# Optimization experiments

Hardware: AMD Instinct MI355X
Metric: run time of the kernel (lower is better)

## Reference

```python
import jax, jax.numpy as jnp
import numpy as np

D_MODEL, D_KEY, N_HEADS = 256, 32, 8
B, T1, T2 = 4, 2048, 2048


def setup_inputs() -> dict:
    key = jax.random.key(0)
    ks = jax.random.split(key, 12)
    s = 1.0 / np.sqrt(D_MODEL)
    inp = {
        "key_input": jax.random.normal(ks[0], (B, T1, D_MODEL), jnp.float32),
        "query_input": jax.random.normal(ks[1], (B, T2, D_MODEL), jnp.float32),
        "value_input": jax.random.normal(ks[2], (B, T1, D_MODEL), jnp.float32),
        "attention_mask": jnp.ones((B, T1, T2), dtype=jnp.bool_),  # unused by the module, kept for API fidelity
        "WK_w": jax.random.uniform(ks[3], (D_KEY * N_HEADS, D_MODEL), jnp.float32, -s, s),
        "WK_b": jax.random.uniform(ks[4], (D_KEY * N_HEADS,), jnp.float32, -s, s),
        "WQ_w": jax.random.uniform(ks[5], (D_KEY * N_HEADS, D_MODEL), jnp.float32, -s, s),
        "WQ_b": jax.random.uniform(ks[6], (D_KEY * N_HEADS,), jnp.float32, -s, s),
        "WV_w": jax.random.uniform(ks[7], (D_MODEL * N_HEADS, D_MODEL), jnp.float32, -s, s),
        "WV_b": jax.random.uniform(ks[8], (D_MODEL * N_HEADS,), jnp.float32, -s, s),
        "WO_w": jax.random.uniform(ks[9], (D_MODEL, D_MODEL * N_HEADS), jnp.float32, -1.0 / np.sqrt(D_MODEL * N_HEADS), 1.0 / np.sqrt(D_MODEL * N_HEADS)),
        "WO_b": jax.random.uniform(ks[10], (D_MODEL,), jnp.float32, -1.0 / np.sqrt(D_MODEL * N_HEADS), 1.0 / np.sqrt(D_MODEL * N_HEADS)),
    }
    return inp


def reference(key_input, query_input, value_input, attention_mask,
              WK_w, WK_b, WQ_w, WQ_b, WV_w, WV_b, WO_w, WO_b):
    b, t1, dm = key_input.shape
    t2 = query_input.shape[1]
    h, dk = N_HEADS, D_KEY
    # projections
    k = key_input @ WK_w.T + WK_b      # [b, t1, h*dk]
    q = query_input @ WQ_w.T + WQ_b    # [b, t2, h*dk]
    v = value_input @ WV_w.T + WV_b    # [b, t1, h*dm] (per-head value dim == d_model)
    # head split: channel index c = head*dk + feat (head outer), matching torch reshapes
    k = k.reshape(b, t1, h, dk)
    q = q.reshape(b, t2, h, dk)
    v = v.reshape(b, t1, h, dm)
    # scores: NO 1/sqrt(dk) scaling and NO masking (faithful to source; mask arg unused)
    scores = jnp.einsum('bshk,bqhk->bhsq', k, q)      # [b, h, t1, t2]
    attn = jax.nn.softmax(scores, axis=2)             # softmax over KEY axis (torch dim=1 of [t1,t2])
    emb = jnp.einsum('bshd,bhsq->bqdh', v, attn)      # [b, t2, dm, h]
    emb = emb.reshape(b, t2, dm * h)                  # flatten (d_model outer, head inner)
    return emb @ WO_w.T + WO_b                        # [b, t2, d_model]
```

## Files before the change

### kernel.cpp

```cpp
#include <hip/hip_runtime.h>

typedef __attribute__((ext_vector_type(8))) short short8;
typedef __attribute__((ext_vector_type(4))) short short4v;
typedef __attribute__((ext_vector_type(4))) float float4v;

constexpr int T  = 2048;
constexpr int DM = 256;
constexpr int DK = 32;

__device__ inline short f2bf(float f) {
  unsigned u = __builtin_bit_cast(unsigned, f);
  u += 0x7fff + ((u >> 16) & 1);
  return (short)(u >> 16);
}

__device__ inline short8 load8_bf(const float* __restrict__ p) {
  float4v a = *(const float4v*)p;
  float4v b = *(const float4v*)(p + 4);
  short8 r;
  r[0] = f2bf(a[0]); r[1] = f2bf(a[1]); r[2] = f2bf(a[2]); r[3] = f2bf(a[3]);
  r[4] = f2bf(b[0]); r[5] = f2bf(b[1]); r[6] = f2bf(b[2]); r[7] = f2bf(b[3]);
  return r;
}
__device__ inline short8 load8_bf(const short* __restrict__ p) {
  return *(const short8*)p;
}
__device__ inline void storeC(short* C, long idx, float v) { C[idx] = f2bf(v); }
__device__ inline void storeC(float* C, long idx, float v) { C[idx] = v; }

template<typename TA, typename TB, typename TC, int MODE>
__global__ __launch_bounds__(256)
void gemm_nt(const TA* __restrict__ A, const TB* __restrict__ Bw,
             const float* __restrict__ bias, TC* __restrict__ C,
             int M, int N, int K) {
  __shared__ __align__(16) short As[128][40];
  __shared__ __align__(16) short Bs[128][40];

  const int tid  = threadIdx.x;
  const int wave = tid >> 6, lane = tid & 63;
  const int l15  = lane & 15, quad = lane >> 4;
  const int wm   = (wave & 1) * 64, wn = (wave >> 1) * 64;
  const long Abase = (long)blockIdx.x * 128;
  const long Bbase = (long)blockIdx.y * 128;

  float4v acc[4][4];
  for (int i = 0; i < 4; i++)
    for (int j = 0; j < 4; j++)
      for (int r = 0; r < 4; r++) acc[i][j][r] = 0.f;

  const int srow = tid >> 2;
  const int sc8  = (tid & 3) * 8;

  for (int k0 = 0; k0 < K; k0 += 32) {
    __syncthreads();
    for (int i = 0; i < 2; i++) {
      int row = srow + i * 64;
      *(short8*)&As[row][sc8] = load8_bf(A  + (Abase + row) * K + k0 + sc8);
      *(short8*)&Bs[row][sc8] = load8_bf(Bw + (Bbase + row) * K + k0 + sc8);
    }
    __syncthreads();
    short8 af[4], bfr[4];
    for (int ms = 0; ms < 4; ms++) af[ms]  = *(const short8*)&As[wm + ms*16 + l15][quad*8];
    for (int ns = 0; ns < 4; ns++) bfr[ns] = *(const short8*)&Bs[wn + ns*16 + l15][quad*8];
    for (int ms = 0; ms < 4; ms++)
      for (int ns = 0; ns < 4; ns++)
        acc[ms][ns] = __builtin_amdgcn_mfma_f32_16x16x32_bf16(af[ms], bfr[ns], acc[ms][ns], 0, 0, 0);
  }

  for (int ms = 0; ms < 4; ms++) {
    int rowl = wm + ms*16 + quad*4;
    for (int ns = 0; ns < 4; ns++) {
      int col = (int)Bbase + wn + ns*16 + l15;
      if (MODE == 0) {
        float bv = bias[col];
        for (int r = 0; r < 4; r++) {
          long row = Abase + rowl + r;
          storeC(C, row * (long)N + col, acc[ms][ns][r] + bv);
        }
      } else {
        int bidx = col >> 11, scol = col & 2047;
        for (int r = 0; r < 4; r++) {
          long m = Abase + rowl + r;
          storeC(C, ((long)bidx * 2048 + m) * 2048 + scol, acc[ms][ns][r] + bias[m]);
        }
      }
    }
  }
}

template<typename TA, typename TB, typename TC, bool DUAL>
__global__ __launch_bounds__(256)
void gemm_nt64(const TA* __restrict__ A, const TB* __restrict__ Bw,
               const float* __restrict__ bias, TC* __restrict__ C,
               const TA* __restrict__ A1, const TB* __restrict__ Bw1,
               const float* __restrict__ bias1, TC* __restrict__ C1,
               float scale1, int M, int N, int K) {
  __shared__ __align__(16) short As[128][40];
  __shared__ __align__(16) short Bs[64][40];

  float oscale = 1.0f;
  if (DUAL && blockIdx.z == 1) { A = A1; Bw = Bw1; bias = bias1; C = C1; oscale = scale1; }

  const int tid  = threadIdx.x;
  const int wave = tid >> 6, lane = tid & 63;
  const int l15  = lane & 15, quad = lane >> 4;
  const int wm   = (wave & 1) * 64, wn = (wave >> 1) * 32;
  const long Abase = (long)blockIdx.x * 128;
  const long Bbase = (long)blockIdx.y * 64;

  float4v acc[4][2];
  for (int i = 0; i < 4; i++)
    for (int j = 0; j < 2; j++)
      for (int r = 0; r < 4; r++) acc[i][j][r] = 0.f;

  const int srow = tid >> 2;
  const int sc8  = (tid & 3) * 8;

  for (int k0 = 0; k0 < K; k0 += 32) {
    __syncthreads();
    for (int i = 0; i < 2; i++) {
      int row = srow + i * 64;
      *(short8*)&As[row][sc8] = load8_bf(A + (Abase + row) * K + k0 + sc8);
    }
    *(short8*)&Bs[srow][sc8] = load8_bf(Bw + (Bbase + srow) * K + k0 + sc8);
    __syncthreads();
    short8 af[4], bfr[2];
    for (int ms = 0; ms < 4; ms++) af[ms]  = *(const short8*)&As[wm + ms*16 + l15][quad*8];
    for (int ns = 0; ns < 2; ns++) bfr[ns] = *(const short8*)&Bs[wn + ns*16 + l15][quad*8];
    for (int ms = 0; ms < 4; ms++)
      for (int ns = 0; ns < 2; ns++)
        acc[ms][ns] = __builtin_amdgcn_mfma_f32_16x16x32_bf16(af[ms], bfr[ns], acc[ms][ns], 0, 0, 0);
  }

  for (int ms = 0; ms < 4; ms++) {
    int rowl = wm + ms*16 + quad*4;
    for (int ns = 0; ns < 2; ns++) {
      int col = (int)Bbase + wn + ns*16 + l15;
      float bv = bias[col];
      for (int r = 0; r < 4; r++) {
        long row = Abase + rowl + r;
        storeC(C, row * (long)N + col, (acc[ms][ns][r] + bv) * oscale);
      }
    }
  }
}

__global__ void permute_wo(const float* __restrict__ src, float* __restrict__ dst) {
  int idx = blockIdx.x * 256 + threadIdx.x;
  int n = idx >> 11, c = idx & 2047;
  int h = c >> 8, d = c & 255;
  dst[idx] = src[n * 2048 + d * 8 + h];
}

__global__ __launch_bounds__(256, 2)
void attn_kernel(const short* __restrict__ Kp, const short* __restrict__ Qp,
                 const short* __restrict__ Vt, short* __restrict__ emb) {
  __shared__ __align__(16) short Pt[2][128][136];
  __shared__ __align__(16) float psum[128][4];

  const int tid  = threadIdx.x;
  const int wave = tid >> 6, lane = tid & 63;
  const int l15  = lane & 15, quad = lane >> 4;

  const int L  = blockIdx.x;
  const int h  = L & 7;
  const int b  = (L >> 3) & 3;
  const int q0 = (L >> 5) * 128;

  const short* Kbh = Kp + (long)b * T * DM + h * DK;
  const short* Qbh = Qp + (long)b * T * DM + h * DK;
  const short* Vbh = Vt + ((long)b * 2048 + h * 256) * 2048;

  float4v acc[4][8];
  for (int i = 0; i < 4; i++)
    for (int j = 0; j < 8; j++)
      for (int r = 0; r < 4; r++) acc[i][j][r] = 0.f;

  float ps[8];
  for (int i = 0; i < 8; i++) ps[i] = 0.f;

  short8 qf[8];
  for (int qs = 0; qs < 8; qs++)
    qf[qs] = *(const short8*)(Qbh + (long)(q0 + qs*16 + l15) * DM + quad*8);

  auto computeSt = [&](int s0, int buf) {
    for (int ss = 0; ss < 2; ss++) {
      short8 kf = *(const short8*)(Kbh + (long)(s0 + wave*32 + ss*16 + l15) * DM + quad*8);
      for (int qs = 0; qs < 8; qs++) {
        float4v z = {0.f, 0.f, 0.f, 0.f};
        float4v st = __builtin_amdgcn_mfma_f32_16x16x32_bf16(kf, qf[qs], z, 0, 0, 0);
        short4v pb;
        float s4 = 0.f;
        for (int r = 0; r < 4; r++) {
          float p = exp2f(st[r]);
          s4 += p;
          pb[r] = f2bf(p);
        }
        ps[qs] += s4;
        *(short4v*)&Pt[buf][qs*16 + l15][wave*32 + ss*16 + quad*4] = pb;
      }
    }
  };

  computeSt(0, 0);

  for (int it = 0; it < T / 128; it++) {
    const int buf = it & 1;
    const int s0  = it * 128;
    __syncthreads();
    if (it < T / 128 - 1) computeSt(s0 + 128, buf ^ 1);
    for (int ks = 0; ks < 4; ks++) {
      short8 pf[8];
      for (int ns = 0; ns < 8; ns++)
        pf[ns] = *(const short8*)&Pt[buf][ns*16 + l15][ks*32 + quad*8];
      for (int ms = 0; ms < 4; ms++) {
        short8 vf = *(const short8*)(Vbh + (long)(wave*64 + ms*16 + l15) * 2048
                                     + s0 + ks*32 + quad*8);
        for (int ns = 0; ns < 8; ns++)
          acc[ms][ns] = __builtin_amdgcn_mfma_f32_16x16x32_bf16(vf, pf[ns], acc[ms][ns], 0, 0, 0);
      }
    }
  }

  for (int qs = 0; qs < 8; qs++) {
    ps[qs] += __shfl_xor(ps[qs], 16, 64);
    ps[qs] += __shfl_xor(ps[qs], 32, 64);
  }
  if (lane < 16)
    for (int qs = 0; qs < 8; qs++) psum[qs*16 + lane][wave] = ps[qs];
  __syncthreads();

  for (int ns = 0; ns < 8; ns++) {
    float4v sv = *(const float4v*)&psum[ns*16 + l15][0];
    float rl = 1.0f / (sv[0] + sv[1] + sv[2] + sv[3]);
    long rowbase = ((long)(b * T + q0 + ns*16 + l15)) * 2048 + h * 256;
    for (int ms = 0; ms < 4; ms++) {
      short4v ob;
      for (int r = 0; r < 4; r++) ob[r] = f2bf(acc[ms][ns][r] * rl);
      *(short4v*)(emb + rowbase + wave*64 + ms*16 + quad*4) = ob;
    }
  }
}

extern "C" void kernel_launch(void* const* d_in, const int* in_sizes, int n_in,
                              void* d_out, int out_size, void* d_ws, size_t ws_size,
                              hipStream_t stream) {
  const float* key_x   = (const float*)d_in[0];
  const float* query_x = (const float*)d_in[1];
  const float* value_x = (const float*)d_in[2];
  const float* WK_w = (const float*)d_in[4];
  const float* WK_b = (const float*)d_in[5];
  const float* WQ_w = (const float*)d_in[6];
  const float* WQ_b = (const float*)d_in[7];
  const float* WV_w = (const float*)d_in[8];
  const float* WV_b = (const float*)d_in[9];
  const float* WO_w = (const float*)d_in[10];
  const float* WO_b = (const float*)d_in[11];

  char* ws = (char*)d_ws;
  short* Kp   = (short*)(ws);
  short* Qp   = (short*)(ws + (4u  << 20));
  short* Vt   = (short*)(ws + (8u  << 20));
  short* embp = (short*)(ws + (40u << 20));
  float* WOp  = (float*)(ws + (72u << 20));
  float* outp = (float*)d_out;

  const float L2E = 1.44269504f;

  permute_wo<<<2048, 256, 0, stream>>>(WO_w, WOp);
  gemm_nt64<float, float, short, true><<<dim3(64, 4, 2), 256, 0, stream>>>(
      key_x, WK_w, WK_b, Kp, query_x, WQ_w, WQ_b, Qp, L2E, 8192, 256, 256);
  gemm_nt<float, float, short, 1><<<dim3(16, 64), 256, 0, stream>>>(
      WV_w, value_x, WV_b, Vt, 2048, 8192, 256);
  attn_kernel<<<dim3(512), 256, 0, stream>>>(Kp, Qp, Vt, embp);
  gemm_nt64<short, float, float, false><<<dim3(64, 4), 256, 0, stream>>>(
      embp, WOp, WO_b, outp, (const short*)nullptr, (const float*)nullptr,
      (const float*)nullptr, (float*)nullptr, 1.0f, 8192, 256, 2048);
}
```

Measured before the change: 330.3 us.

## Split-K output GEMM with atomics, packed bf16 converts, single-buffer attention P tile

```diff
diff --git a/kernel.cpp b/kernel.cpp
--- a/kernel.cpp
+++ b/kernel.cpp
@@ -3,6 +3,8 @@
 typedef __attribute__((ext_vector_type(8))) short short8;
 typedef __attribute__((ext_vector_type(4))) short short4v;
 typedef __attribute__((ext_vector_type(4))) float float4v;
+typedef __attribute__((ext_vector_type(4))) unsigned uint4v;
+typedef __attribute__((ext_vector_type(2))) unsigned uint2v;
 
 constexpr int T  = 2048;
 constexpr int DM = 256;
@@ -14,13 +16,26 @@
   return (short)(u >> 16);
 }
 
+__device__ inline unsigned pk2(float a, float b) {
+#if __has_builtin(__builtin_amdgcn_cvt_pk_bf16_f32)
+  auto r = __builtin_amdgcn_cvt_pk_bf16_f32(a, b);
+  return __builtin_bit_cast(unsigned, r);
+#else
+  unsigned ua = __builtin_bit_cast(unsigned, a);
+  ua = (ua + 0x7fff + ((ua >> 16) & 1)) >> 16;
+  unsigned ub = __builtin_bit_cast(unsigned, b);
+  ub = (ub + 0x7fff + ((ub >> 16) & 1)) >> 16;
+  return ua | (ub << 16);
+#endif
+}
+
 __device__ inline short8 load8_bf(const float* __restrict__ p) {
   float4v a = *(const float4v*)p;
   float4v b = *(const float4v*)(p + 4);
-  short8 r;
-  r[0] = f2bf(a[0]); r[1] = f2bf(a[1]); r[2] = f2bf(a[2]); r[3] = f2bf(a[3]);
-  r[4] = f2bf(b[0]); r[5] = f2bf(b[1]); r[6] = f2bf(b[2]); r[7] = f2bf(b[3]);
-  return r;
+  uint4v u;
+  u[0] = pk2(a[0], a[1]); u[1] = pk2(a[2], a[3]);
+  u[2] = pk2(b[0], b[1]); u[3] = pk2(b[2], b[3]);
+  return __builtin_bit_cast(short8, u);
 }
 __device__ inline short8 load8_bf(const short* __restrict__ p) {
   return *(const short8*)p;
@@ -145,6 +160,62 @@
   }
 }
 
+__global__ __launch_bounds__(256)
+void gemm_sk(const short* __restrict__ A, const float* __restrict__ Bw,
+             float* __restrict__ C) {
+  __shared__ __align__(16) short As[128][40];
+  __shared__ __align__(16) short Bs[64][40];
+
+  const int tid  = threadIdx.x;
+  const int wave = tid >> 6, lane = tid & 63;
+  const int l15  = lane & 15, quad = lane >> 4;
+  const int wm   = (wave & 1) * 64, wn = (wave >> 1) * 32;
+  const long Abase = (long)blockIdx.x * 128;
+  const long Bbase = (long)blockIdx.y * 64;
+  const int  kbase = blockIdx.z * 1024;
+  const int  N = 256, K = 2048;
+
+  float4v acc[4][2];
+  for (int i = 0; i < 4; i++)
+    for (int j = 0; j < 2; j++)
+      for (int r = 0; r < 4; r++) acc[i][j][r] = 0.f;
+
+  const int srow = tid >> 2;
+  const int sc8  = (tid & 3) * 8;
+
+  for (int k0 = kbase; k0 < kbase + 1024; k0 += 32) {
+    __syncthreads();
+    for (int i = 0; i < 2; i++) {
+      int row = srow + i * 64;
+      *(short8*)&As[row][sc8] = load8_bf(A + (Abase + row) * K + k0 + sc8);
+    }
+    *(short8*)&Bs[srow][sc8] = load8_bf(Bw + (Bbase + srow) * K + k0 + sc8);
+    __syncthreads();
+    short8 af[4], bfr[2];
+    for (int ms = 0; ms < 4; ms++) af[ms]  = *(const short8*)&As[wm + ms*16 + l15][quad*8];
+    for (int ns = 0; ns < 2; ns++) bfr[ns] = *(const short8*)&Bs[wn + ns*16 + l15][quad*8];
+    for (int ms = 0; ms < 4; ms++)
+      for (int ns = 0; ns < 2; ns++)
+        acc[ms][ns] = __builtin_amdgcn_mfma_f32_16x16x32_bf16(af[ms], bfr[ns], acc[ms][ns], 0, 0, 0);
+  }
+
+  for (int ms = 0; ms < 4; ms++) {
+    int rowl = wm + ms*16 + quad*4;
+    for (int ns = 0; ns < 2; ns++) {
+      int col = (int)Bbase + wn + ns*16 + l15;
+      for (int r = 0; r < 4; r++) {
+        long row = Abase + rowl + r;
+        atomicAdd(&C[row * (long)N + col], acc[ms][ns][r]);
+      }
+    }
+  }
+}
+
+__global__ void bias_fill(const float* __restrict__ b, float* __restrict__ out) {
+  int idx = blockIdx.x * 256 + threadIdx.x;
+  out[idx] = b[idx & 255];
+}
+
 __global__ void permute_wo(const float* __restrict__ src, float* __restrict__ dst) {
   int idx = blockIdx.x * 256 + threadIdx.x;
   int n = idx >> 11, c = idx & 2047;
@@ -155,7 +226,7 @@
 __global__ __launch_bounds__(256, 2)
 void attn_kernel(const short* __restrict__ Kp, const short* __restrict__ Qp,
                  const short* __restrict__ Vt, short* __restrict__ emb) {
-  __shared__ __align__(16) short Pt[2][128][136];
+  __shared__ __align__(16) short Pt[128][136];
   __shared__ __align__(16) float psum[128][4];
 
   const int tid  = threadIdx.x;
@@ -183,36 +254,27 @@
   for (int qs = 0; qs < 8; qs++)
     qf[qs] = *(const short8*)(Qbh + (long)(q0 + qs*16 + l15) * DM + quad*8);
 
-  auto computeSt = [&](int s0, int buf) {
+  for (int it = 0; it < T / 128; it++) {
+    const int s0 = it * 128;
+
     for (int ss = 0; ss < 2; ss++) {
       short8 kf = *(const short8*)(Kbh + (long)(s0 + wave*32 + ss*16 + l15) * DM + quad*8);
       for (int qs = 0; qs < 8; qs++) {
         float4v z = {0.f, 0.f, 0.f, 0.f};
         float4v st = __builtin_amdgcn_mfma_f32_16x16x32_bf16(kf, qf[qs], z, 0, 0, 0);
-        short4v pb;
-        float s4 = 0.f;
-        for (int r = 0; r < 4; r++) {
-          float p = exp2f(st[r]);
-          s4 += p;
-          pb[r] = f2bf(p);
-        }
-        ps[qs] += s4;
-        *(short4v*)&Pt[buf][qs*16 + l15][wave*32 + ss*16 + quad*4] = pb;
-      }
-    }
-  };
-
-  computeSt(0, 0);
-
-  for (int it = 0; it < T / 128; it++) {
-    const int buf = it & 1;
-    const int s0  = it * 128;
-    __syncthreads();
-    if (it < T / 128 - 1) computeSt(s0 + 128, buf ^ 1);
+        float p0 = exp2f(st[0]), p1 = exp2f(st[1]);
+        float p2 = exp2f(st[2]), p3 = exp2f(st[3]);
+        ps[qs] += (p0 + p1) + (p2 + p3);
+        uint2v pb; pb[0] = pk2(p0, p1); pb[1] = pk2(p2, p3);
+        *(uint2v*)&Pt[qs*16 + l15][wave*32 + ss*16 + quad*4] = pb;
+      }
+    }
+    __syncthreads();
+
     for (int ks = 0; ks < 4; ks++) {
       short8 pf[8];
       for (int ns = 0; ns < 8; ns++)
-        pf[ns] = *(const short8*)&Pt[buf][ns*16 + l15][ks*32 + quad*8];
+        pf[ns] = *(const short8*)&Pt[ns*16 + l15][ks*32 + quad*8];
       for (int ms = 0; ms < 4; ms++) {
         short8 vf = *(const short8*)(Vbh + (long)(wave*64 + ms*16 + l15) * 2048
                                      + s0 + ks*32 + quad*8);
@@ -220,6 +282,7 @@
           acc[ms][ns] = __builtin_amdgcn_mfma_f32_16x16x32_bf16(vf, pf[ns], acc[ms][ns], 0, 0, 0);
       }
     }
+    __syncthreads();
   }
 
   for (int qs = 0; qs < 8; qs++) {
@@ -235,9 +298,10 @@
     float rl = 1.0f / (sv[0] + sv[1] + sv[2] + sv[3]);
     long rowbase = ((long)(b * T + q0 + ns*16 + l15)) * 2048 + h * 256;
     for (int ms = 0; ms < 4; ms++) {
-      short4v ob;
-      for (int r = 0; r < 4; r++) ob[r] = f2bf(acc[ms][ns][r] * rl);
-      *(short4v*)(emb + rowbase + wave*64 + ms*16 + quad*4) = ob;
+      uint2v ob;
+      ob[0] = pk2(acc[ms][ns][0] * rl, acc[ms][ns][1] * rl);
+      ob[1] = pk2(acc[ms][ns][2] * rl, acc[ms][ns][3] * rl);
+      *(uint2v*)(emb + rowbase + wave*64 + ms*16 + quad*4) = ob;
     }
   }
 }
@@ -273,7 +337,6 @@
   gemm_nt<float, float, short, 1><<<dim3(16, 64), 256, 0, stream>>>(
       WV_w, value_x, WV_b, Vt, 2048, 8192, 256);
   attn_kernel<<<dim3(512), 256, 0, stream>>>(Kp, Qp, Vt, embp);
-  gemm_nt64<short, float, float, false><<<dim3(64, 4), 256, 0, stream>>>(
-      embp, WOp, WO_b, outp, (const short*)nullptr, (const float*)nullptr,
-      (const float*)nullptr, (float*)nullptr, 1.0f, 8192, 256, 2048);
-}
+  bias_fill<<<8192, 256, 0, stream>>>(WO_b, outp);
+  gemm_sk<<<dim3(64, 4, 2), 256, 0, stream>>>(embp, WOp, outp);
+}
```

Result: slower. 346.9 us (+5.0%).
